# Optimization experiments

Measured on AMD Instinct MI355X. Metric: run time of the kernel, lower is better.

Reference implementation:

```python
import jax, jax.numpy as jnp
import numpy as np

N, E = 50000, 800000
F_IN, H, OUT, L = 32, 128, 20, 4


def setup_inputs() -> dict:
    key = jax.random.key(0)
    ks = jax.random.split(key, 32)
    s = 0.05  # weight scale
    inp = {
        "h": jax.random.normal(ks[0], (N, F_IN), jnp.float32),
        "x": jax.random.normal(ks[1], (N, 3), jnp.float32),
        "edges": jax.random.randint(ks[2], (2, E), 0, N, jnp.int32),
        # embeddings
        "emb_in_w": jax.random.normal(ks[3], (F_IN, H)) * s,
        "emb_in_b": jnp.zeros((H,)),
        "emb_out_w": jax.random.normal(ks[4], (H, H)) * s,
        "emb_out_b": jnp.zeros((H,)),
        # per-layer stacked params
        "edge_w1": jax.random.normal(ks[5], (L, 2 * H + 1, H)) * s,
        "edge_b1": jnp.zeros((L, H)),
        "edge_w2": jax.random.normal(ks[6], (L, H, H)) * s,
        "edge_b2": jnp.zeros((L, H)),
        "att_w": jax.random.normal(ks[7], (L, H, 1)) * s,
        "att_b": jnp.zeros((L, 1)),
        "coord_w1": jax.random.normal(ks[8], (L, H, H)) * s,
        "coord_b1": jnp.zeros((L, H)),
        "coord_w2": jax.random.normal(ks[9], (L, H, 1)) * s,  # no bias (egnn_clean)
        "node_w1": jax.random.normal(ks[10], (L, 2 * H, H)) * s,
        "node_b1": jnp.zeros((L, H)),
        "node_w2": jax.random.normal(ks[11], (L, H, H)) * s,
        "node_b2": jnp.zeros((L, H)),
        # head MLP
        "head_w1": jax.random.normal(ks[12], (H, H)) * s,
        "head_b1": jnp.zeros((H,)),
        "head_w2": jax.random.normal(ks[13], (H, OUT)) * s,
        "head_b2": jnp.zeros((OUT,)),
    }
    return inp


def reference(h, x, edges, emb_in_w, emb_in_b, emb_out_w, emb_out_b,
              edge_w1, edge_b1, edge_w2, edge_b2, att_w, att_b,
              coord_w1, coord_b1, coord_w2,
              node_w1, node_b1, node_w2, node_b2,
              head_w1, head_b1, head_w2, head_b2):
    n = h.shape[0]
    row, col = edges[0], edges[1]
    h = h @ emb_in_w + emb_in_b
    for l in range(L):
        diff = x[row] - x[col]                       # [E,3]
        radial = jnp.sum(diff * diff, -1, keepdims=True)  # [E,1]
        m = jnp.concatenate([h[row], h[col], radial], -1)  # [E,2H+1]
        m = jax.nn.silu(m @ edge_w1[l] + edge_b1[l])
        m = jax.nn.silu(m @ edge_w2[l] + edge_b2[l])
        m = m * jax.nn.sigmoid(m @ att_w[l] + att_b[l])  # attention gate
        # coordinate update: segment mean of diff * coord_mlp(m)
        cw = jax.nn.silu(m @ coord_w1[l] + coord_b1[l]) @ coord_w2[l]  # [E,1]
        trans = diff * cw
        agg_x = jax.ops.segment_sum(trans, row, num_segments=n)
        cnt = jax.ops.segment_sum(jnp.ones((E, 1), trans.dtype), row, num_segments=n)
        x = x + agg_x / jnp.maximum(cnt, 1.0)
        # node update: residual MLP on [h, segment_sum(m)]
        agg_m = jax.ops.segment_sum(m, row, num_segments=n)
        hcat = jnp.concatenate([h, agg_m], -1)
        h = h + (jax.nn.silu(hcat @ node_w1[l] + node_b1[l]) @ node_w2[l] + node_b2[l])
    h = h @ emb_out_w + emb_out_b
    g = jnp.mean(h, axis=0)  # mean pool over nodes
    out = jax.nn.relu(g @ head_w1 + head_b1) @ head_w2 + head_b2
    return out[None, :]  # [1, OUT]
```

## Files before the change

kernel.cpp:

```cpp
#include <hip/hip_runtime.h>
#include <hip/hip_bf16.h>

#define NN   50000
#define EE   800000
#define FIN  32
#define HH   128
#define LL   4
#define NOUT 20

typedef __attribute__((ext_vector_type(8))) short bf16x8;
typedef __attribute__((ext_vector_type(4))) short short4v;
typedef __attribute__((ext_vector_type(4))) float f32x4;

__device__ __forceinline__ float silu_f(float v){ return v / (1.f + __expf(-v)); }
__device__ __forceinline__ float sigm_f(float v){ return 1.f / (1.f + __expf(-v)); }

__device__ __forceinline__ short f2bf(float v){
  union { float f; unsigned u; } a; a.f = v;
  unsigned r = a.u + 0x7fff + ((a.u >> 16) & 1);
  return (short)(r >> 16);
}
__device__ __forceinline__ float bf2f(short s){
  union { unsigned u; float f; } a; a.u = ((unsigned)(unsigned short)s) << 16;
  return a.f;
}

__device__ __forceinline__ f32x4 mfma16(bf16x8 a, bf16x8 b, f32x4 c){
  return __builtin_amdgcn_mfma_f32_16x16x32_bf16(a, b, c, 0, 0, 0);
}

__device__ __forceinline__ void gemm_mfma(const short* Ah, const short* Al,
                                          const float* __restrict__ W,
                                          int lane, int wc0, f32x4 acc[4][2])
{
  const int cl = lane & 15, g = lane >> 4;
  bf16x8 Bh[4][2], Bl[4][2];
  #pragma unroll
  for (int kb = 0; kb < 4; kb++) {
    #pragma unroll
    for (int cf = 0; cf < 2; cf++) {
      const float* wp = W + (size_t)(kb*32 + g*8)*HH + wc0 + cf*16 + cl;
      bf16x8 hv, lv;
      #pragma unroll
      for (int j = 0; j < 8; j++) {
        const float v = wp[(size_t)j*HH];
        const short hh = f2bf(v);
        const short ll = f2bf(v - bf2f(hh));
        hv[j] = hh; lv[j] = ll;
      }
      Bh[kb][cf] = hv; Bl[kb][cf] = lv;
    }
  }
  #pragma unroll
  for (int kb = 0; kb < 4; kb++) {
    #pragma unroll
    for (int fr = 0; fr < 4; fr++) {
      const int e = fr*16 + cl;
      const int off = e*128 + ((kb*32 + g*8) ^ ((e&7)<<3));
      const bf16x8 ah = *(const bf16x8*)&Ah[off];
      const bf16x8 al = *(const bf16x8*)&Al[off];
      #pragma unroll
      for (int cf = 0; cf < 2; cf++) {
        acc[fr][cf] = mfma16(ah, Bh[kb][cf], acc[fr][cf]);
        acc[fr][cf] = mfma16(ah, Bl[kb][cf], acc[fr][cf]);
        acc[fr][cf] = mfma16(al, Bh[kb][cf], acc[fr][cf]);
      }
    }
  }
}

__device__ __forceinline__ void stage_h(const float* __restrict__ hsrc, const int* idx,
                                        short* Ah, short* Al, int tid)
{
  const int l32 = tid & 31, hgr = tid >> 5;
  const int c4 = l32 * 4;
  #pragma unroll
  for (int j = 0; j < 8; j++) {
    const int e = hgr + 8*j;
    const float4 v = *(const float4*)&hsrc[(size_t)idx[e]*HH + c4];
    short4v hv, lv;
    hv.x = f2bf(v.x); lv.x = f2bf(v.x - bf2f(hv.x));
    hv.y = f2bf(v.y); lv.y = f2bf(v.y - bf2f(hv.y));
    hv.z = f2bf(v.z); lv.z = f2bf(v.z - bf2f(hv.z));
    hv.w = f2bf(v.w); lv.w = f2bf(v.w - bf2f(hv.w));
    const int o = e*128 + (c4 ^ ((e&7)<<3));
    *(short4v*)&Ah[o] = hv;
    *(short4v*)&Al[o] = lv;
  }
}

__global__ __launch_bounds__(256)
void k_embed(const float* __restrict__ hin, const float* __restrict__ xin,
             const float* __restrict__ W, const float* __restrict__ b,
             float* __restrict__ hout, float* __restrict__ xout)
{
  __shared__ float wl[FIN*HH];
  const int tid = threadIdx.x;
  for (int j = tid; j < FIN*HH; j += 256) wl[j] = W[j];
  __syncthreads();
  const int c  = tid & (HH-1);
  const int no = tid >> 7;
  const int v  = blockIdx.x * 2 + no;
  if (v < NN) {
    const float* hr = hin + (size_t)v * FIN;
    float acc = b[c];
    #pragma unroll
    for (int k = 0; k < FIN; k++) acc = fmaf(hr[k], wl[k*HH + c], acc);
    hout[(size_t)v*HH + c] = acc;
    if (c < 3) xout[v*3 + c] = xin[v*3 + c];
  }
}

__global__ __launch_bounds__(256)
void k_count(const int* __restrict__ row, int* __restrict__ deg)
{
  const int e = blockIdx.x * 256 + threadIdx.x;
  if (e < EE) atomicAdd(&deg[row[e]], 1);
}

__global__ __launch_bounds__(1024)
void k_scan(const int* __restrict__ deg, int* __restrict__ offs, int* __restrict__ cursor)
{
  __shared__ int part[1024];
  const int t = threadIdx.x;
  const int base = t * 49;
  int s = 0;
  for (int i = 0; i < 49; i++) { const int idx = base + i; s += (idx < NN) ? deg[idx] : 0; }
  part[t] = s;
  __syncthreads();
  if (t == 0) { int run = 0; for (int i = 0; i < 1024; i++) { const int v = part[i]; part[i] = run; run += v; } }
  __syncthreads();
  int run = part[t];
  for (int i = 0; i < 49; i++) {
    const int idx = base + i;
    if (idx < NN) { offs[idx] = run; cursor[idx] = run; run += deg[idx]; }
  }
  if (t == 1023) offs[NN] = EE;
}

__global__ __launch_bounds__(256)
void k_pos(const int* __restrict__ row, int* __restrict__ cursor, int* __restrict__ pos)
{
  const int e = blockIdx.x * 256 + threadIdx.x;
  if (e < EE) pos[e] = atomicAdd(&cursor[row[e]], 1);
}

template<bool SC>
__global__ __launch_bounds__(256)
void k_edge(const float* __restrict__ hbuf, const float* __restrict__ xbuf,
            const int* __restrict__ row, const int* __restrict__ col,
            const int* __restrict__ pos,
            const float* __restrict__ W1, const float* __restrict__ b1,
            const float* __restrict__ W2, const float* __restrict__ b2,
            const float* __restrict__ attw, const float* __restrict__ attb,
            const float* __restrict__ cw1, const float* __restrict__ cb1,
            const float* __restrict__ cw2,
            float* __restrict__ mbuf, float* __restrict__ aggx)
{
  __shared__ short Ah[64*128];
  __shared__ short Al[64*128];
  __shared__ float red[4][64];
  __shared__ float scal[64];
  __shared__ int   rowb[64];
  __shared__ int   colb[64];
  __shared__ int   posb[64];
  __shared__ float diffb[64][3];
  __shared__ float radb[64];

  const int tid  = threadIdx.x;
  const int lane = tid & 63;
  const int wv   = tid >> 6;
  const int cl   = lane & 15;
  const int g    = lane >> 4;
  const int wc0  = wv * 32;
  const int col0 = wc0 + cl;
  const int col1 = wc0 + 16 + cl;
  const int eb   = blockIdx.x * 64;

  if (tid < 64) {
    const int r  = row[eb + tid];
    const int c2 = col[eb + tid];
    rowb[tid] = r; colb[tid] = c2;
    if (SC) posb[tid] = pos[eb + tid];
    const float dx = xbuf[r*3+0] - xbuf[c2*3+0];
    const float dy = xbuf[r*3+1] - xbuf[c2*3+1];
    const float dz = xbuf[r*3+2] - xbuf[c2*3+2];
    diffb[tid][0] = dx; diffb[tid][1] = dy; diffb[tid][2] = dz;
    radb[tid] = dx*dx + dy*dy + dz*dz;
  }
  __syncthreads();

  stage_h(hbuf, rowb, Ah, Al, tid);
  __syncthreads();

  f32x4 acc[4][2];
  #pragma unroll
  for (int fr = 0; fr < 4; fr++) { acc[fr][0] = (f32x4){0,0,0,0}; acc[fr][1] = (f32x4){0,0,0,0}; }
  gemm_mfma(Ah, Al, W1, lane, wc0, acc);
  __syncthreads();

  stage_h(hbuf, colb, Ah, Al, tid);
  __syncthreads();

  gemm_mfma(Ah, Al, W1 + HH*HH, lane, wc0, acc);

  {
    const float w256a = W1[(size_t)(2*HH)*HH + col0];
    const float w256b = W1[(size_t)(2*HH)*HH + col1];
    const float bba = b1[col0], bbb = b1[col1];
    #pragma unroll
    for (int fr = 0; fr < 4; fr++) {
      #pragma unroll
      for (int j = 0; j < 4; j++) {
        const int r = fr*16 + g*4 + j;
        const float rr = radb[r];
        acc[fr][0][j] = silu_f(fmaf(rr, w256a, acc[fr][0][j]) + bba);
        acc[fr][1][j] = silu_f(fmaf(rr, w256b, acc[fr][1][j]) + bbb);
      }
    }
  }
  __syncthreads();

  #pragma unroll
  for (int fr = 0; fr < 4; fr++) {
    #pragma unroll
    for (int j = 0; j < 4; j++) {
      const int r = fr*16 + g*4 + j;
      const int sw = (r&7)<<3;
      const float v0 = acc[fr][0][j], v1 = acc[fr][1][j];
      const short h0 = f2bf(v0), h1 = f2bf(v1);
      Ah[r*128 + (col0 ^ sw)] = h0;  Al[r*128 + (col0 ^ sw)] = f2bf(v0 - bf2f(h0));
      Ah[r*128 + (col1 ^ sw)] = h1;  Al[r*128 + (col1 ^ sw)] = f2bf(v1 - bf2f(h1));
    }
  }
  __syncthreads();

  f32x4 m2[4][2];
  #pragma unroll
  for (int fr = 0; fr < 4; fr++) { m2[fr][0] = (f32x4){0,0,0,0}; m2[fr][1] = (f32x4){0,0,0,0}; }
  gemm_mfma(Ah, Al, W2, lane, wc0, m2);
  {
    const float bba = b2[col0], bbb = b2[col1];
    #pragma unroll
    for (int fr = 0; fr < 4; fr++) {
      #pragma unroll
      for (int j = 0; j < 4; j++) {
        m2[fr][0][j] = silu_f(m2[fr][0][j] + bba);
        m2[fr][1][j] = silu_f(m2[fr][1][j] + bbb);
      }
    }
  }

  {
    const float awa = attw[col0], awb = attw[col1];
    #pragma unroll
    for (int fr = 0; fr < 4; fr++) {
      #pragma unroll
      for (int j = 0; j < 4; j++) {
        float p = fmaf(m2[fr][0][j], awa, m2[fr][1][j]*awb);
        p += __shfl_xor(p, 1); p += __shfl_xor(p, 2);
        p += __shfl_xor(p, 4); p += __shfl_xor(p, 8);
        if (cl == 0) red[wv][fr*16 + g*4 + j] = p;
      }
    }
  }
  __syncthreads();
  if (tid < 64)
    scal[tid] = sigm_f(red[0][tid] + red[1][tid] + red[2][tid] + red[3][tid] + attb[0]);
  __syncthreads();

  #pragma unroll
  for (int fr = 0; fr < 4; fr++) {
    #pragma unroll
    for (int j = 0; j < 4; j++) {
      const int r = fr*16 + g*4 + j;
      const float sc = scal[r];
      const float v0 = m2[fr][0][j]*sc, v1 = m2[fr][1][j]*sc;
      m2[fr][0][j] = v0; m2[fr][1][j] = v1;
      if (SC) {
        float* dst = &mbuf[(size_t)posb[r]*HH];
        dst[col0] = v0; dst[col1] = v1;
      } else {
        float* dst = &mbuf[(size_t)rowb[r]*HH];
        atomicAdd(&dst[col0], v0); atomicAdd(&dst[col1], v1);
      }
      const int sw = (r&7)<<3;
      const short h0 = f2bf(v0), h1 = f2bf(v1);
      Ah[r*128 + (col0 ^ sw)] = h0;  Al[r*128 + (col0 ^ sw)] = f2bf(v0 - bf2f(h0));
      Ah[r*128 + (col1 ^ sw)] = h1;  Al[r*128 + (col1 ^ sw)] = f2bf(v1 - bf2f(h1));
    }
  }
  __syncthreads();

  f32x4 a3[4][2];
  #pragma unroll
  for (int fr = 0; fr < 4; fr++) { a3[fr][0] = (f32x4){0,0,0,0}; a3[fr][1] = (f32x4){0,0,0,0}; }
  gemm_mfma(Ah, Al, cw1, lane, wc0, a3);
  {
    const float bba = cb1[col0], bbb = cb1[col1];
    const float c2a = cw2[col0], c2b = cw2[col1];
    #pragma unroll
    for (int fr = 0; fr < 4; fr++) {
      #pragma unroll
      for (int j = 0; j < 4; j++) {
        float p = fmaf(silu_f(a3[fr][0][j] + bba), c2a, silu_f(a3[fr][1][j] + bbb)*c2b);
        p += __shfl_xor(p, 1); p += __shfl_xor(p, 2);
        p += __shfl_xor(p, 4); p += __shfl_xor(p, 8);
        if (cl == 0) red[wv][fr*16 + g*4 + j] = p;
      }
    }
  }
  __syncthreads();

  if (tid < 64) {
    const float cwv = red[0][tid] + red[1][tid] + red[2][tid] + red[3][tid];
    const int r = rowb[tid];
    atomicAdd(&aggx[r*3+0], diffb[tid][0]*cwv);
    atomicAdd(&aggx[r*3+1], diffb[tid][1]*cwv);
    atomicAdd(&aggx[r*3+2], diffb[tid][2]*cwv);
  }
}

__device__ __forceinline__ void gemm_accum(const float (*buf)[132], const float* __restrict__ W,
                                           int c, int eo, float acc[32])
{
  for (int k0 = 0; k0 < HH; k0 += 4) {
    const float w0 = W[(k0+0)*HH + c];
    const float w1 = W[(k0+1)*HH + c];
    const float w2 = W[(k0+2)*HH + c];
    const float w3 = W[(k0+3)*HH + c];
    #pragma unroll
    for (int i = 0; i < 32; i++) {
      const float4 a = *(const float4*)&buf[eo*32+i][k0];
      acc[i] = fmaf(a.x, w0, fmaf(a.y, w1, fmaf(a.z, w2, fmaf(a.w, w3, acc[i]))));
    }
  }
}

template<bool SC>
__global__ __launch_bounds__(256, 2)
void k_node(float* __restrict__ hbuf, float* __restrict__ xbuf,
            const float* __restrict__ mbuf, const int* __restrict__ offs,
            const float* __restrict__ aggx,
            const float* __restrict__ W1, const float* __restrict__ b1,
            const float* __restrict__ W2, const float* __restrict__ b2)
{
  __shared__ float bufA[64][132];
  __shared__ float bufB[64][132];
  const int tid = threadIdx.x;
  const int c   = tid & (HH-1);
  const int no  = tid >> 7;
  const int nb  = blockIdx.x * 64;

  #pragma unroll
  for (int i = 0; i < 32; i++) {
    const int v = nb + no*32 + i;
    bufA[no*32+i][c] = (v < NN) ? hbuf[(size_t)v*HH + c] : 0.f;
  }
  __syncthreads();

  float acc[32];
  #pragma unroll
  for (int i = 0; i < 32; i++) acc[i] = 0.f;
  gemm_accum(bufA, W1, c, no, acc);
  __syncthreads();

  for (int i = 0; i < 32; i++) {
    const int v = nb + no*32 + i;
    float s = 0.f;
    if (v < NN) {
      if (SC) {
        const int beg = offs[v], end = offs[v+1];
        for (int j = beg; j < end; j++) s += mbuf[(size_t)j*HH + c];
      } else {
        s = mbuf[(size_t)v*HH + c];
      }
    }
    bufA[no*32+i][c] = s;
  }
  __syncthreads();
  gemm_accum(bufA, W1 + HH*HH, c, no, acc);
  {
    const float bb = b1[c];
    #pragma unroll
    for (int i = 0; i < 32; i++) bufB[no*32+i][c] = silu_f(acc[i] + bb);
  }
  __syncthreads();

  #pragma unroll
  for (int i = 0; i < 32; i++) acc[i] = 0.f;
  gemm_accum(bufB, W2, c, no, acc);
  {
    const float bb = b2[c];
    #pragma unroll
    for (int i = 0; i < 32; i++) {
      const int v = nb + no*32 + i;
      if (v < NN) hbuf[(size_t)v*HH + c] += acc[i] + bb;
    }
  }

  if (tid < 64) {
    const int v = nb + tid;
    if (v < NN) {
      const float ct = fmaxf((float)(offs[v+1] - offs[v]), 1.f);
      xbuf[v*3+0] += aggx[v*3+0] / ct;
      xbuf[v*3+1] += aggx[v*3+1] / ct;
      xbuf[v*3+2] += aggx[v*3+2] / ct;
    }
  }
}

__global__ __launch_bounds__(128)
void k_pool(const float* __restrict__ h, float* __restrict__ g)
{
  const int c  = threadIdx.x;
  const int v0 = blockIdx.x * 100;
  float s = 0.f;
  for (int v = v0; v < v0 + 100; ++v) s += h[(size_t)v*HH + c];
  atomicAdd(&g[c], s);
}

__global__ __launch_bounds__(128)
void k_head(const float* __restrict__ g,
            const float* __restrict__ eow, const float* __restrict__ eob,
            const float* __restrict__ hw1, const float* __restrict__ hb1,
            const float* __restrict__ hw2, const float* __restrict__ hb2,
            float* __restrict__ out)
{
  __shared__ float gm[HH], ho[HH], t1[HH];
  const int c = threadIdx.x;
  gm[c] = g[c] * (1.f / (float)NN);
  __syncthreads();
  float a = eob[c];
  for (int k = 0; k < HH; k++) a = fmaf(gm[k], eow[k*HH + c], a);
  ho[c] = a;
  __syncthreads();
  float t = hb1[c];
  for (int k = 0; k < HH; k++) t = fmaf(ho[k], hw1[k*HH + c], t);
  t1[c] = fmaxf(t, 0.f);
  __syncthreads();
  if (c < NOUT) {
    float o = hb2[c];
    for (int k = 0; k < HH; k++) o = fmaf(t1[k], hw2[k*NOUT + c], o);
    out[c] = o;
  }
}

extern "C" void kernel_launch(void* const* d_in, const int* in_sizes, int n_in,
                              void* d_out, int out_size, void* d_ws, size_t ws_size,
                              hipStream_t stream)
{
  const float* in_h  = (const float*)d_in[0];
  const float* in_x  = (const float*)d_in[1];
  const int*   edges = (const int*)  d_in[2];
  const float* eiw   = (const float*)d_in[3];
  const float* eib   = (const float*)d_in[4];
  const float* eow   = (const float*)d_in[5];
  const float* eob   = (const float*)d_in[6];
  const float* ew1   = (const float*)d_in[7];
  const float* eb1   = (const float*)d_in[8];
  const float* ew2   = (const float*)d_in[9];
  const float* eb2   = (const float*)d_in[10];
  const float* attw  = (const float*)d_in[11];
  const float* attb  = (const float*)d_in[12];
  const float* cw1   = (const float*)d_in[13];
  const float* cb1   = (const float*)d_in[14];
  const float* cw2   = (const float*)d_in[15];
  const float* nw1   = (const float*)d_in[16];
  const float* nb1   = (const float*)d_in[17];
  const float* nw2   = (const float*)d_in[18];
  const float* nb2   = (const float*)d_in[19];
  const float* hw1   = (const float*)d_in[20];
  const float* hb1   = (const float*)d_in[21];
  const float* hw2   = (const float*)d_in[22];
  const float* hb2   = (const float*)d_in[23];

  const int* row = edges;
  const int* col = edges + EE;

  char* p = (char*)d_ws;
  auto alloc = [&](size_t bytes) { char* r = p; p += (bytes + 255) & ~(size_t)255; return r; };
  float* h    = (float*)alloc((size_t)NN*HH*4);
  float* x    = (float*)alloc((size_t)NN*3*4);
  float* aggx = (float*)alloc((size_t)NN*3*4);
  float* g    = (float*)alloc(HH*4);
  int*   deg  = (int*)  alloc((size_t)NN*4);
  int*   offs = (int*)  alloc((size_t)(NN+1)*4);
  int*   curs = (int*)  alloc((size_t)NN*4);
  int*   pos  = (int*)  alloc((size_t)EE*4);
  const size_t baseUsed = (size_t)(p - (char*)d_ws);
  const bool sc = (ws_size >= baseUsed + (size_t)EE*HH*4);
  float* mbuf = (float*)alloc(sc ? (size_t)EE*HH*4 : (size_t)NN*HH*4);

  k_embed<<<NN/2, 256, 0, stream>>>(in_h, in_x, eiw, eib, h, x);

  hipMemsetAsync(deg, 0, (size_t)NN*4, stream);
  k_count<<<(EE+255)/256, 256, 0, stream>>>(row, deg);
  k_scan<<<1, 1024, 0, stream>>>(deg, offs, curs);
  k_pos<<<(EE+255)/256, 256, 0, stream>>>(row, curs, pos);

  for (int l = 0; l < LL; l++) {
    hipMemsetAsync(aggx, 0, (size_t)NN*3*4, stream);
    if (!sc) hipMemsetAsync(mbuf, 0, (size_t)NN*HH*4, stream);
    if (sc) {
      k_edge<true><<<EE/64, 256, 0, stream>>>(h, x, row, col, pos,
          ew1 + (size_t)l*(2*HH+1)*HH, eb1 + l*HH,
          ew2 + (size_t)l*HH*HH,       eb2 + l*HH,
          attw + l*HH, attb + l,
          cw1 + (size_t)l*HH*HH, cb1 + l*HH, cw2 + l*HH,
          mbuf, aggx);
      k_node<true><<<(NN + 63)/64, 256, 0, stream>>>(h, x, mbuf, offs, aggx,
          nw1 + (size_t)l*(2*HH)*HH, nb1 + l*HH,
          nw2 + (size_t)l*HH*HH,     nb2 + l*HH);
    } else {
      k_edge<false><<<EE/64, 256, 0, stream>>>(h, x, row, col, pos,
          ew1 + (size_t)l*(2*HH+1)*HH, eb1 + l*HH,
          ew2 + (size_t)l*HH*HH,       eb2 + l*HH,
          attw + l*HH, attb + l,
          cw1 + (size_t)l*HH*HH, cb1 + l*HH, cw2 + l*HH,
          mbuf, aggx);
      k_node<false><<<(NN + 63)/64, 256, 0, stream>>>(h, x, mbuf, offs, aggx,
          nw1 + (size_t)l*(2*HH)*HH, nb1 + l*HH,
          nw2 + (size_t)l*HH*HH,     nb2 + l*HH);
    }
  }

  hipMemsetAsync(g, 0, HH*4, stream);
  k_pool<<<500, 128, 0, stream>>>(h, g);
  k_head<<<1, 128, 0, stream>>>(g, eow, eob, hw1, hb1, hw2, hb2, (float*)d_out);
}
```

Baseline: 3.845 ms.

## Precompute bf16 hi/lo splits of weights and node features once per layer

A new prep kernel converts the edge and coord MLP weights into transposed bf16 hi/lo pairs once, so the edge kernel loads ready-made MFMA B fragments with vector loads instead of converting strided fp32 weights in every block. The node features are likewise stored as bf16 hi/lo arrays by the embed and node kernels, so gathering rows in the edge kernel becomes a plain bf16 copy with no per-edge conversion. This removes a large amount of repeated conversion ALU work and halves the gather width per array, at the cost of extra workspace and extra writes in the node kernel.

```diff
diff --git a/kernel.cpp b/kernel.cpp
--- a/kernel.cpp
+++ b/kernel.cpp
@@ -30,69 +30,80 @@
 }
 
 __device__ __forceinline__ void gemm_mfma(const short* Ah, const short* Al,
-                                          const float* __restrict__ W,
+                                          const short* __restrict__ Wh,
+                                          const short* __restrict__ Wl,
                                           int lane, int wc0, f32x4 acc[4][2])
 {
   const int cl = lane & 15, g = lane >> 4;
-  bf16x8 Bh[4][2], Bl[4][2];
+  const int wb0 = (wc0 + cl)*HH + g*8;
+  const int wb1 = (wc0 + 16 + cl)*HH + g*8;
   #pragma unroll
   for (int kb = 0; kb < 4; kb++) {
-    #pragma unroll
-    for (int cf = 0; cf < 2; cf++) {
-      const float* wp = W + (size_t)(kb*32 + g*8)*HH + wc0 + cf*16 + cl;
-      bf16x8 hv, lv;
-      #pragma unroll
-      for (int j = 0; j < 8; j++) {
-        const float v = wp[(size_t)j*HH];
-        const short hh = f2bf(v);
-        const short ll = f2bf(v - bf2f(hh));
-        hv[j] = hh; lv[j] = ll;
-      }
-      Bh[kb][cf] = hv; Bl[kb][cf] = lv;
-    }
-  }
-  #pragma unroll
-  for (int kb = 0; kb < 4; kb++) {
+    const int kk = kb*32 + g*8;
+    bf16x8 bh[2], bl[2];
+    bh[0] = *(const bf16x8*)&Wh[wb0 + kb*32];
+    bl[0] = *(const bf16x8*)&Wl[wb0 + kb*32];
+    bh[1] = *(const bf16x8*)&Wh[wb1 + kb*32];
+    bl[1] = *(const bf16x8*)&Wl[wb1 + kb*32];
     #pragma unroll
     for (int fr = 0; fr < 4; fr++) {
       const int e = fr*16 + cl;
-      const int off = e*128 + ((kb*32 + g*8) ^ ((e&7)<<3));
+      const int off = e*128 + (kk ^ ((e&7)<<3));
       const bf16x8 ah = *(const bf16x8*)&Ah[off];
       const bf16x8 al = *(const bf16x8*)&Al[off];
       #pragma unroll
       for (int cf = 0; cf < 2; cf++) {
-        acc[fr][cf] = mfma16(ah, Bh[kb][cf], acc[fr][cf]);
-        acc[fr][cf] = mfma16(ah, Bl[kb][cf], acc[fr][cf]);
-        acc[fr][cf] = mfma16(al, Bh[kb][cf], acc[fr][cf]);
-      }
-    }
-  }
-}
-
-__device__ __forceinline__ void stage_h(const float* __restrict__ hsrc, const int* idx,
-                                        short* Ah, short* Al, int tid)
-{
-  const int l32 = tid & 31, hgr = tid >> 5;
-  const int c4 = l32 * 4;
-  #pragma unroll
-  for (int j = 0; j < 8; j++) {
-    const int e = hgr + 8*j;
-    const float4 v = *(const float4*)&hsrc[(size_t)idx[e]*HH + c4];
-    short4v hv, lv;
-    hv.x = f2bf(v.x); lv.x = f2bf(v.x - bf2f(hv.x));
-    hv.y = f2bf(v.y); lv.y = f2bf(v.y - bf2f(hv.y));
-    hv.z = f2bf(v.z); lv.z = f2bf(v.z - bf2f(hv.z));
-    hv.w = f2bf(v.w); lv.w = f2bf(v.w - bf2f(hv.w));
-    const int o = e*128 + (c4 ^ ((e&7)<<3));
-    *(short4v*)&Ah[o] = hv;
-    *(short4v*)&Al[o] = lv;
+        acc[fr][cf] = mfma16(ah, bh[cf], acc[fr][cf]);
+        acc[fr][cf] = mfma16(ah, bl[cf], acc[fr][cf]);
+        acc[fr][cf] = mfma16(al, bh[cf], acc[fr][cf]);
+      }
+    }
+  }
+}
+
+__device__ __forceinline__ void stage_p(const short* __restrict__ hbi,
+                                        const short* __restrict__ hlo,
+                                        const int* idx, short* Ah, short* Al, int tid)
+{
+  const int e = tid >> 2;
+  const int q = tid & 3;
+  const int base = idx[e]*HH;
+  #pragma unroll
+  for (int u = 0; u < 4; u++) {
+    const int c = q*8 + u*32;
+    const int o = e*128 + (c ^ ((e&7)<<3));
+    *(bf16x8*)&Ah[o] = *(const bf16x8*)&hbi[base + c];
+    *(bf16x8*)&Al[o] = *(const bf16x8*)&hlo[base + c];
+  }
+}
+
+__global__ __launch_bounds__(256)
+void k_prep(const float* __restrict__ ew1, const float* __restrict__ ew2,
+            const float* __restrict__ cw1v, short* __restrict__ wph,
+            short* __restrict__ wpl)
+{
+  const int b = blockIdx.x;
+  const int l = b >> 2, m = b & 3;
+  const float* src = (m==0) ? ew1 + (size_t)l*(2*HH+1)*HH
+                   : (m==1) ? ew1 + (size_t)l*(2*HH+1)*HH + HH*HH
+                   : (m==2) ? ew2 + (size_t)l*HH*HH
+                            : cw1v + (size_t)l*HH*HH;
+  short* dh = wph + (size_t)b*HH*HH;
+  short* dl = wpl + (size_t)b*HH*HH;
+  for (int idx = threadIdx.x; idx < HH*HH; idx += 256) {
+    const int k = idx >> 7, c = idx & 127;
+    const float v = src[idx];
+    const short hh = f2bf(v);
+    dh[c*HH + k] = hh;
+    dl[c*HH + k] = f2bf(v - bf2f(hh));
   }
 }
 
 __global__ __launch_bounds__(256)
 void k_embed(const float* __restrict__ hin, const float* __restrict__ xin,
              const float* __restrict__ W, const float* __restrict__ b,
-             float* __restrict__ hout, float* __restrict__ xout)
+             float* __restrict__ hout, float* __restrict__ xout,
+             short* __restrict__ hbi, short* __restrict__ hlo)
 {
   __shared__ float wl[FIN*HH];
   const int tid = threadIdx.x;
@@ -107,6 +118,9 @@
     #pragma unroll
     for (int k = 0; k < FIN; k++) acc = fmaf(hr[k], wl[k*HH + c], acc);
     hout[(size_t)v*HH + c] = acc;
+    const short hh = f2bf(acc);
+    hbi[(size_t)v*HH + c] = hh;
+    hlo[(size_t)v*HH + c] = f2bf(acc - bf2f(hh));
     if (c < 3) xout[v*3 + c] = xin[v*3 + c];
   }
 }
@@ -147,14 +161,15 @@
 
 template<bool SC>
 __global__ __launch_bounds__(256)
-void k_edge(const float* __restrict__ hbuf, const float* __restrict__ xbuf,
+void k_edge(const short* __restrict__ hbi, const short* __restrict__ hlo,
+            const float* __restrict__ xbuf,
             const int* __restrict__ row, const int* __restrict__ col,
             const int* __restrict__ pos,
+            const short* __restrict__ wph, const short* __restrict__ wpl, int lidx,
             const float* __restrict__ W1, const float* __restrict__ b1,
-            const float* __restrict__ W2, const float* __restrict__ b2,
+            const float* __restrict__ b2,
             const float* __restrict__ attw, const float* __restrict__ attb,
-            const float* __restrict__ cw1, const float* __restrict__ cb1,
-            const float* __restrict__ cw2,
+            const float* __restrict__ cb1, const float* __restrict__ cw2,
             float* __restrict__ mbuf, float* __restrict__ aggx)
 {
   __shared__ short Ah[64*128];
@@ -176,6 +191,15 @@
   const int col0 = wc0 + cl;
   const int col1 = wc0 + 16 + cl;
   const int eb   = blockIdx.x * 64;
+
+  const short* W1a_h = wph + (size_t)(lidx*4+0)*HH*HH;
+  const short* W1a_l = wpl + (size_t)(lidx*4+0)*HH*HH;
+  const short* W1b_h = wph + (size_t)(lidx*4+1)*HH*HH;
+  const short* W1b_l = wpl + (size_t)(lidx*4+1)*HH*HH;
+  const short* W2_h  = wph + (size_t)(lidx*4+2)*HH*HH;
+  const short* W2_l  = wpl + (size_t)(lidx*4+2)*HH*HH;
+  const short* C1_h  = wph + (size_t)(lidx*4+3)*HH*HH;
+  const short* C1_l  = wpl + (size_t)(lidx*4+3)*HH*HH;
 
   if (tid < 64) {
     const int r  = row[eb + tid];
@@ -190,19 +214,19 @@
   }
   __syncthreads();
 
-  stage_h(hbuf, rowb, Ah, Al, tid);
+  stage_p(hbi, hlo, rowb, Ah, Al, tid);
   __syncthreads();
 
   f32x4 acc[4][2];
   #pragma unroll
   for (int fr = 0; fr < 4; fr++) { acc[fr][0] = (f32x4){0,0,0,0}; acc[fr][1] = (f32x4){0,0,0,0}; }
-  gemm_mfma(Ah, Al, W1, lane, wc0, acc);
-  __syncthreads();
-
-  stage_h(hbuf, colb, Ah, Al, tid);
-  __syncthreads();
-
-  gemm_mfma(Ah, Al, W1 + HH*HH, lane, wc0, acc);
+  gemm_mfma(Ah, Al, W1a_h, W1a_l, lane, wc0, acc);
+  __syncthreads();
+
+  stage_p(hbi, hlo, colb, Ah, Al, tid);
+  __syncthreads();
+
+  gemm_mfma(Ah, Al, W1b_h, W1b_l, lane, wc0, acc);
 
   {
     const float w256a = W1[(size_t)(2*HH)*HH + col0];
@@ -238,7 +262,7 @@
   f32x4 m2[4][2];
   #pragma unroll
   for (int fr = 0; fr < 4; fr++) { m2[fr][0] = (f32x4){0,0,0,0}; m2[fr][1] = (f32x4){0,0,0,0}; }
-  gemm_mfma(Ah, Al, W2, lane, wc0, m2);
+  gemm_mfma(Ah, Al, W2_h, W2_l, lane, wc0, m2);
   {
     const float bba = b2[col0], bbb = b2[col1];
     #pragma unroll
@@ -276,7 +300,6 @@
       const int r = fr*16 + g*4 + j;
       const float sc = scal[r];
       const float v0 = m2[fr][0][j]*sc, v1 = m2[fr][1][j]*sc;
-      m2[fr][0][j] = v0; m2[fr][1][j] = v1;
       if (SC) {
         float* dst = &mbuf[(size_t)posb[r]*HH];
         dst[col0] = v0; dst[col1] = v1;
@@ -295,7 +318,7 @@
   f32x4 a3[4][2];
   #pragma unroll
   for (int fr = 0; fr < 4; fr++) { a3[fr][0] = (f32x4){0,0,0,0}; a3[fr][1] = (f32x4){0,0,0,0}; }
-  gemm_mfma(Ah, Al, cw1, lane, wc0, a3);
+  gemm_mfma(Ah, Al, C1_h, C1_l, lane, wc0, a3);
   {
     const float bba = cb1[col0], bbb = cb1[col1];
     const float c2a = cw2[col0], c2b = cw2[col1];
@@ -343,7 +366,8 @@
             const float* __restrict__ mbuf, const int* __restrict__ offs,
             const float* __restrict__ aggx,
             const float* __restrict__ W1, const float* __restrict__ b1,
-            const float* __restrict__ W2, const float* __restrict__ b2)
+            const float* __restrict__ W2, const float* __restrict__ b2,
+            short* __restrict__ hbi, short* __restrict__ hlo)
 {
   __shared__ float bufA[64][132];
   __shared__ float bufB[64][132];
@@ -395,7 +419,13 @@
     #pragma unroll
     for (int i = 0; i < 32; i++) {
       const int v = nb + no*32 + i;
-      if (v < NN) hbuf[(size_t)v*HH + c] += acc[i] + bb;
+      if (v < NN) {
+        const float hn = hbuf[(size_t)v*HH + c] + acc[i] + bb;
+        hbuf[(size_t)v*HH + c] = hn;
+        const short hh = f2bf(hn);
+        hbi[(size_t)v*HH + c] = hh;
+        hlo[(size_t)v*HH + c] = f2bf(hn - bf2f(hh));
+      }
     }
   }
 
@@ -488,11 +518,16 @@
   int*   offs = (int*)  alloc((size_t)(NN+1)*4);
   int*   curs = (int*)  alloc((size_t)NN*4);
   int*   pos  = (int*)  alloc((size_t)EE*4);
+  short* hbi  = (short*)alloc((size_t)NN*HH*2);
+  short* hlo  = (short*)alloc((size_t)NN*HH*2);
+  short* wph  = (short*)alloc((size_t)16*HH*HH*2);
+  short* wpl  = (short*)alloc((size_t)16*HH*HH*2);
   const size_t baseUsed = (size_t)(p - (char*)d_ws);
   const bool sc = (ws_size >= baseUsed + (size_t)EE*HH*4);
   float* mbuf = (float*)alloc(sc ? (size_t)EE*HH*4 : (size_t)NN*HH*4);
 
-  k_embed<<<NN/2, 256, 0, stream>>>(in_h, in_x, eiw, eib, h, x);
+  k_prep<<<16, 256, 0, stream>>>(ew1, ew2, cw1, wph, wpl);
+  k_embed<<<NN/2, 256, 0, stream>>>(in_h, in_x, eiw, eib, h, x, hbi, hlo);
 
   hipMemsetAsync(deg, 0, (size_t)NN*4, stream);
   k_count<<<(EE+255)/256, 256, 0, stream>>>(row, deg);
@@ -503,25 +538,23 @@
     hipMemsetAsync(aggx, 0, (size_t)NN*3*4, stream);
     if (!sc) hipMemsetAsync(mbuf, 0, (size_t)NN*HH*4, stream);
     if (sc) {
-      k_edge<true><<<EE/64, 256, 0, stream>>>(h, x, row, col, pos,
-          ew1 + (size_t)l*(2*HH+1)*HH, eb1 + l*HH,
-          ew2 + (size_t)l*HH*HH,       eb2 + l*HH,
-          attw + l*HH, attb + l,
-          cw1 + (size_t)l*HH*HH, cb1 + l*HH, cw2 + l*HH,
+      k_edge<true><<<EE/64, 256, 0, stream>>>(hbi, hlo, x, row, col, pos,
+          wph, wpl, l,
+          ew1 + (size_t)l*(2*HH+1)*HH, eb1 + l*HH, eb2 + l*HH,
+          attw + l*HH, attb + l, cb1 + l*HH, cw2 + l*HH,
           mbuf, aggx);
       k_node<true><<<(NN + 63)/64, 256, 0, stream>>>(h, x, mbuf, offs, aggx,
           nw1 + (size_t)l*(2*HH)*HH, nb1 + l*HH,
-          nw2 + (size_t)l*HH*HH,     nb2 + l*HH);
+          nw2 + (size_t)l*HH*HH,     nb2 + l*HH, hbi, hlo);
     } else {
-      k_edge<false><<<EE/64, 256, 0, stream>>>(h, x, row, col, pos,
-          ew1 + (size_t)l*(2*HH+1)*HH, eb1 + l*HH,
-          ew2 + (size_t)l*HH*HH,       eb2 + l*HH,
-          attw + l*HH, attb + l,
-          cw1 + (size_t)l*HH*HH, cb1 + l*HH, cw2 + l*HH,
+      k_edge<false><<<EE/64, 256, 0, stream>>>(hbi, hlo, x, row, col, pos,
+          wph, wpl, l,
+          ew1 + (size_t)l*(2*HH+1)*HH, eb1 + l*HH, eb2 + l*HH,
+          attw + l*HH, attb + l, cb1 + l*HH, cw2 + l*HH,
           mbuf, aggx);
       k_node<false><<<(NN + 63)/64, 256, 0, stream>>>(h, x, mbuf, offs, aggx,
           nw1 + (size_t)l*(2*HH)*HH, nb1 + l*HH,
-          nw2 + (size_t)l*HH*HH,     nb2 + l*HH);
+          nw2 + (size_t)l*HH*HH,     nb2 + l*HH, hbi, hlo);
     }
   }
 
```

After: 4.250 ms. 10.5% more time.
